# Optimization experiments

Hardware: AMD Instinct MI355X
Metric: run time of the kernel (lower is better)

The kernel has to match this reference:

```python
import jax, jax.numpy as jnp
import numpy as np

N_EMBD = 768
N_HEAD = 12
BLOCK_SIZE = 1024


def setup_inputs() -> dict:
    key = jax.random.key(0)
    ks = jax.random.split(key, 11)
    s = lambda fan_in: 1.0 / np.sqrt(fan_in)
    x = jax.random.normal(ks[0], (8, 1024, N_EMBD), dtype=jnp.float32)
    return {
        "x": x,
        "ln1_g": jnp.ones((N_EMBD,), jnp.float32),
        "ln1_b": jnp.zeros((N_EMBD,), jnp.float32),
        "w_attn": jax.random.normal(ks[1], (N_EMBD, 3 * N_EMBD), jnp.float32) * s(N_EMBD),
        "b_attn": jnp.zeros((3 * N_EMBD,), jnp.float32),
        "w_proj": jax.random.normal(ks[2], (N_EMBD, N_EMBD), jnp.float32) * s(N_EMBD),
        "b_proj": jnp.zeros((N_EMBD,), jnp.float32),
        "ln2_g": jnp.ones((N_EMBD,), jnp.float32),
        "ln2_b": jnp.zeros((N_EMBD,), jnp.float32),
        "w_fc": jax.random.normal(ks[3], (N_EMBD, 4 * N_EMBD), jnp.float32) * s(N_EMBD),
        "b_fc": jnp.zeros((4 * N_EMBD,), jnp.float32),
        "w_fc_proj": jax.random.normal(ks[4], (4 * N_EMBD, N_EMBD), jnp.float32) * s(4 * N_EMBD),
        "b_fc_proj": jnp.zeros((N_EMBD,), jnp.float32),
    }


def _layernorm(x, g, b, eps=1e-5):
    mu = jnp.mean(x, axis=-1, keepdims=True)
    var = jnp.var(x, axis=-1, keepdims=True)
    return (x - mu) * jax.lax.rsqrt(var + eps) * g + b


def _gelu_tanh(x):
    # GELU with tanh approximation (matches nn.GELU(approximate='tanh'))
    c = np.sqrt(2.0 / np.pi).astype(np.float32)
    return 0.5 * x * (1.0 + jnp.tanh(c * (x + 0.044715 * x * x * x)))


def _attn(x, w_attn, b_attn, w_proj, b_proj):
    B, T, C = x.shape
    hs = C // N_HEAD
    qkv = x @ w_attn + b_attn  # [B,T,3C]
    q, k, v = jnp.split(qkv, 3, axis=-1)
    # [B,T,C] -> [B,nh,T,hs]
    to_heads = lambda t: t.reshape(B, T, N_HEAD, hs).transpose(0, 2, 1, 3)
    q, k, v = to_heads(q), to_heads(k), to_heads(v)
    att = jnp.einsum('bhqd,bhkd->bhqk', q, k) * (1.0 / np.sqrt(hs))
    causal = jnp.tril(jnp.ones((T, T), bool))
    att = jnp.where(causal, att, -jnp.inf)
    att = jax.nn.softmax(att, axis=-1)
    y = jnp.einsum('bhqk,bhkd->bhqd', att, v)  # [B,nh,T,hs]
    y = y.transpose(0, 2, 1, 3).reshape(B, T, C)
    return y @ w_proj + b_proj


def reference(x, ln1_g, ln1_b, w_attn, b_attn, w_proj, b_proj,
              ln2_g, ln2_b, w_fc, b_fc, w_fc_proj, b_fc_proj):
    x = x + _attn(_layernorm(x, ln1_g, ln1_b), w_attn, b_attn, w_proj, b_proj)
    h = _layernorm(x, ln2_g, ln2_b)
    h = _gelu_tanh(h @ w_fc + b_fc) @ w_fc_proj + b_fc_proj
    return x + h
```

## Files before the change

### kernel.cpp

```cpp
#include <hip/hip_runtime.h>

typedef __bf16 bf16x8 __attribute__((ext_vector_type(8)));
typedef float  f32x4  __attribute__((ext_vector_type(4)));
typedef unsigned short ushort8 __attribute__((ext_vector_type(8)));

__device__ __forceinline__ unsigned short f2bf(float f) {
    unsigned u = __float_as_uint(f);
    u += 0x7FFFu + ((u >> 16) & 1u);
    return (unsigned short)(u >> 16);
}

__device__ __forceinline__ f32x4 mfma16x16x32(bf16x8 a, bf16x8 b, f32x4 c) {
    return __builtin_amdgcn_mfma_f32_16x16x32_bf16(a, b, c, 0, 0, 0);
}

__device__ __forceinline__ bf16x8 ld8(const unsigned short* p) {
    return __builtin_bit_cast(bf16x8, *(const ushort8*)p);
}

__device__ __forceinline__ float exp2_fast(float x) {
    float r; asm("v_exp_f32 %0, %1" : "=v"(r) : "v"(x)); return r;
}

__device__ __forceinline__ void glds16(const unsigned short* g, unsigned short* l) {
    __builtin_amdgcn_global_load_lds(
        (const __attribute__((address_space(1))) void*)g,
        (__attribute__((address_space(3))) void*)l, 16, 0, 0);
}

__device__ __forceinline__ float gelu_tanh(float x) {
    const float c = 0.7978845608028654f;
    float z = c * (x + 0.044715f * x * x * x);
    float e = __expf(2.f * z);
    float th = 1.f - 2.f / (e + 1.f);
    return 0.5f * x * (1.f + th);
}

#define N_EMBD 768
#define SEQ    1024
#define NHEAD  12
#define HS     64
#define MROWS  8192

__global__ __launch_bounds__(256) void tcast_kernel(const float* __restrict__ in,
                                                    unsigned short* __restrict__ out,
                                                    int K, int N) {
    __shared__ float tile[32][33];
    int nb = blockIdx.x * 32, kb = blockIdx.y * 32;
    int tx = threadIdx.x, ty = threadIdx.y;
#pragma unroll
    for (int i = 0; i < 4; i++) {
        int k = kb + ty + i * 8;
        tile[ty + i * 8][tx] = in[(size_t)k * N + nb + tx];
    }
    __syncthreads();
#pragma unroll
    for (int i = 0; i < 4; i++) {
        int n = nb + ty + i * 8;
        out[(size_t)n * K + kb + tx] = f2bf(tile[tx][ty + i * 8]);
    }
}

__global__ __launch_bounds__(256) void ln_kernel(const float* __restrict__ x,
                                                 const float* __restrict__ g,
                                                 const float* __restrict__ b,
                                                 unsigned short* __restrict__ out) {
    int row = blockIdx.x;
    const float* xr = x + (size_t)row * N_EMBD;
    float v[3], s = 0.f, s2 = 0.f;
#pragma unroll
    for (int i = 0; i < 3; i++) {
        v[i] = xr[threadIdx.x + i * 256];
        s += v[i]; s2 += v[i] * v[i];
    }
#pragma unroll
    for (int m = 1; m < 64; m <<= 1) { s += __shfl_xor(s, m); s2 += __shfl_xor(s2, m); }
    __shared__ float ps[4], ps2[4];
    int wid = threadIdx.x >> 6;
    if ((threadIdx.x & 63) == 0) { ps[wid] = s; ps2[wid] = s2; }
    __syncthreads();
    s  = ps[0] + ps[1] + ps[2] + ps[3];
    s2 = ps2[0] + ps2[1] + ps2[2] + ps2[3];
    float mu  = s * (1.f / N_EMBD);
    float var = s2 * (1.f / N_EMBD) - mu * mu;
    float inv = rsqrtf(var + 1e-5f);
#pragma unroll
    for (int i = 0; i < 3; i++) {
        int c = threadIdx.x + i * 256;
        out[(size_t)row * N_EMBD + c] = f2bf((v[i] - mu) * inv * g[c] + b[c]);
    }
}

template <int EPI, int WM>
__global__ __launch_bounds__(256) void gemm_bt_kernel(
    const unsigned short* __restrict__ A, const unsigned short* __restrict__ BT,
    const float* __restrict__ bias, const float* __restrict__ res,
    float* __restrict__ outF, unsigned short* __restrict__ outB,
    int M, int N, int K) {
    constexpr int BM = WM * 32;
    constexpr int ASZ = BM * 64;
    constexpr int BSZ = 128 * 64;
    __shared__ __attribute__((aligned(16))) unsigned short As[2 * ASZ];
    __shared__ __attribute__((aligned(16))) unsigned short Bs[2 * BSZ];
    const int gx = gridDim.x;
    const int slot = blockIdx.y * gx + blockIdx.x;
    const int chunk = (gx * gridDim.y) >> 3;
    const int logical = (slot & 7) * chunk + (slot >> 3);
    const int m0 = (logical / gx) * BM, n0 = (logical % gx) * 128;
    const int t = threadIdx.x, lane = t & 63, wid = t >> 6;
    const int wr = wid >> 1, wc = wid & 1;

    f32x4 acc[WM][4] = {};

    const int rrow = lane & 15, g = lane >> 4;
    const int swz8 = (rrow & 7) << 3;

    const int srow = t >> 3;
    const int scol = ((t & 7) ^ (srow & 7)) * 8;

    const int NT = K >> 6;
#pragma unroll
    for (int i = 0; i < WM; i++)
        glds16(&A[(size_t)(m0 + i * 32 + srow) * K + scol], &As[i * 2048 + wid * 512]);
#pragma unroll
    for (int i = 0; i < 4; i++)
        glds16(&BT[(size_t)(n0 + i * 32 + srow) * K + scol], &Bs[i * 2048 + wid * 512]);
    __syncthreads();

    int cur = 0;
    for (int kt = 0; kt < NT; ++kt) {
        if (kt + 1 < NT) {
            const int kk = (kt + 1) << 6;
            const int nb = (cur ^ 1);
#pragma unroll
            for (int i = 0; i < WM; i++)
                glds16(&A[(size_t)(m0 + i * 32 + srow) * K + kk + scol],
                       &As[nb * ASZ + i * 2048 + wid * 512]);
#pragma unroll
            for (int i = 0; i < 4; i++)
                glds16(&BT[(size_t)(n0 + i * 32 + srow) * K + kk + scol],
                       &Bs[nb * BSZ + i * 2048 + wid * 512]);
        }
        const unsigned short* ab = &As[cur * ASZ];
        const unsigned short* bb = &Bs[cur * BSZ];
#pragma unroll
        for (int s = 0; s < 2; s++) {
            bf16x8 af[WM], bfr[4];
#pragma unroll
            for (int i = 0; i < WM; i++) {
                int row = wr * (WM * 16) + i * 16 + rrow;
                af[i] = ld8(&ab[row * 64 + ((((s << 2) | g) << 3) ^ swz8)]);
            }
#pragma unroll
            for (int j = 0; j < 4; j++) {
                int row = wc * 64 + j * 16 + rrow;
                bfr[j] = ld8(&bb[row * 64 + ((((s << 2) | g) << 3) ^ swz8)]);
            }
#pragma unroll
            for (int i = 0; i < WM; i++)
#pragma unroll
                for (int j = 0; j < 4; j++) acc[i][j] = mfma16x16x32(af[i], bfr[j], acc[i][j]);
        }
        __syncthreads();
        cur ^= 1;
    }

    const int crow = g * 4, ccol = rrow;
#pragma unroll
    for (int i = 0; i < WM; i++) {
        int gr0 = m0 + wr * (WM * 16) + i * 16 + crow;
#pragma unroll
        for (int j = 0; j < 4; j++) {
            int gc = n0 + wc * 64 + j * 16 + ccol;
            float bv = bias[gc];
#pragma unroll
            for (int r = 0; r < 4; r++) {
                int gr = gr0 + r;
                float v = acc[i][j][r] + bv;
                if constexpr (EPI == 1) v = gelu_tanh(v);
                if constexpr (EPI == 2) {
                    outF[(size_t)gr * N + gc] = v + res[(size_t)gr * N + gc];
                } else {
                    outB[(size_t)gr * N + gc] = f2bf(v);
                }
            }
        }
    }
}

#define SCALE_LOG2E 0.18033688011112042f

__global__ __launch_bounds__(256, 4) void attn_kernel(const unsigned short* __restrict__ qkv,
                                                      unsigned short* __restrict__ yb) {
    const int slot = blockIdx.y * 8 + blockIdx.x;
    const int logical = (slot & 7) * 96 + (slot >> 3);
    const int p = logical & 7;
    const int bh = logical >> 3;
    const int b = bh / NHEAD, h = bh % NHEAD;
    const int t = threadIdx.x, lane = t & 63, wid = t >> 6;
    const int q0A = p * 64 + wid * 16, q0B = (15 - p) * 64 + wid * 16;
    const int ntA = p + 1, ntB = 16 - p;
    const int rrow = lane & 15, g = lane >> 4, kg8 = g * 8;

    __shared__ __attribute__((aligned(16))) unsigned short Ks[64 * 64];
    __shared__ __attribute__((aligned(16))) unsigned short Vt[64 * 88];
    __shared__ __attribute__((aligned(16))) unsigned short Ps[4][2][16 * 80];

    bf16x8 qfA[2], qfB[2];
    {
        size_t baseA = ((size_t)(b * SEQ + q0A + rrow)) * 2304 + h * HS;
        qfA[0] = ld8(&qkv[baseA + kg8]);
        qfA[1] = ld8(&qkv[baseA + 32 + kg8]);
        size_t baseB = ((size_t)(b * SEQ + q0B + rrow)) * 2304 + h * HS;
        qfB[0] = ld8(&qkv[baseB + kg8]);
        qfB[1] = ld8(&qkv[baseB + 32 + kg8]);
    }

    f32x4 yA[4] = {}, yB[4] = {};
    float lA[4] = {0.f, 0.f, 0.f, 0.f}, lB[4] = {0.f, 0.f, 0.f, 0.f};

    const int kr0 = t >> 3, kr1 = kr0 + 32;
    const int kc0 = ((t & 7) ^ (kr0 & 7)) * 8;
    const int vd = t & 63, vk = (t >> 6) * 16;

    unsigned short* PB = &Ps[wid][0][0];
    unsigned short* PA = &Ps[wid][1][0];
    const bf16x8 vones = __builtin_bit_cast(bf16x8,
        (ushort8){0x3F80, 0x3F80, 0x3F80, 0x3F80, 0x3F80, 0x3F80, 0x3F80, 0x3F80});

    for (int tt = 0; tt < ntB; tt++) {
        const int kv0 = tt * 64;
        const bool doA = (tt < ntA);
        const bool maskB = (tt == ntB - 1), maskA = (tt == ntA - 1);
        __syncthreads();
        glds16(&qkv[((size_t)(b * SEQ + kv0 + kr0)) * 2304 + 768 + h * HS + kc0], &Ks[wid * 512]);
        glds16(&qkv[((size_t)(b * SEQ + kv0 + kr1)) * 2304 + 768 + h * HS + kc0], &Ks[2048 + wid * 512]);
        ushort8 vlo, vhi;
#pragma unroll
        for (int i = 0; i < 8; i++)
            vlo[i] = qkv[((size_t)(b * SEQ + kv0 + vk + i)) * 2304 + 1536 + h * HS + vd];
#pragma unroll
        for (int i = 0; i < 8; i++)
            vhi[i] = qkv[((size_t)(b * SEQ + kv0 + vk + 8 + i)) * 2304 + 1536 + h * HS + vd];
        *(ushort8*)&Vt[vd * 88 + vk] = vlo;
        *(ushort8*)&Vt[vd * 88 + vk + 8] = vhi;
        __syncthreads();

        f32x4 sB[4], sA[4];
#pragma unroll
        for (int ct = 0; ct < 4; ct++) {
            const int j = ct * 16 + rrow;
            const unsigned short* kr = &Ks[j * 64];
            bf16x8 k0 = ld8(&kr[((g    ) ^ (j & 7)) * 8]);
            bf16x8 k1 = ld8(&kr[((g + 4) ^ (j & 7)) * 8]);
            f32x4 zB = {};
            zB = mfma16x16x32(qfB[0], k0, zB);
            zB = mfma16x16x32(qfB[1], k1, zB);
            sB[ct] = zB;
            if (doA) {
                f32x4 zA = {};
                zA = mfma16x16x32(qfA[0], k0, zA);
                zA = mfma16x16x32(qfA[1], k1, zA);
                sA[ct] = zA;
            }
        }
        const int qrbB = q0B + g * 4, qrbA = q0A + g * 4;
#pragma unroll
        for (int ct = 0; ct < 4; ct++) {
            const int j = ct * 16 + rrow, jj = kv0 + j;
#pragma unroll
            for (int r = 0; r < 4; r++) {
                float v = sB[ct][r] * SCALE_LOG2E;
                if (maskB && jj > qrbB + r) v = -1e30f;
                const int q = g * 4 + r;
                PB[q * 80 + (j ^ ((q & 7) << 3))] = f2bf(exp2_fast(v));
            }
        }
        if (doA) {
#pragma unroll
            for (int ct = 0; ct < 4; ct++) {
                const int j = ct * 16 + rrow, jj = kv0 + j;
#pragma unroll
                for (int r = 0; r < 4; r++) {
                    float v = sA[ct][r] * SCALE_LOG2E;
                    if (maskA && jj > qrbA + r) v = -1e30f;
                    const int q = g * 4 + r;
                    PA[q * 80 + (j ^ ((q & 7) << 3))] = f2bf(exp2_fast(v));
                }
            }
        }
        asm volatile("s_waitcnt lgkmcnt(0)" ::: "memory");
        __builtin_amdgcn_sched_barrier(0);
        const int sw = (rrow & 7) << 3;
        bf16x8 paB0 = ld8(&PB[rrow * 80 + ((kg8     ) ^ sw)]);
        bf16x8 paB1 = ld8(&PB[rrow * 80 + ((kg8 + 32) ^ sw)]);
        bf16x8 paA0, paA1;
        if (doA) {
            paA0 = ld8(&PA[rrow * 80 + ((kg8     ) ^ sw)]);
            paA1 = ld8(&PA[rrow * 80 + ((kg8 + 32) ^ sw)]);
        }
        __builtin_amdgcn_s_setprio(1);
        f32x4 ssB = {};
        ssB = mfma16x16x32(paB0, vones, ssB);
        ssB = mfma16x16x32(paB1, vones, ssB);
#pragma unroll
        for (int r = 0; r < 4; r++) lB[r] += ssB[r];
        if (doA) {
            f32x4 ssA = {};
            ssA = mfma16x16x32(paA0, vones, ssA);
            ssA = mfma16x16x32(paA1, vones, ssA);
#pragma unroll
            for (int r = 0; r < 4; r++) lA[r] += ssA[r];
        }
#pragma unroll
        for (int dt = 0; dt < 4; dt++) {
            const unsigned short* vr = &Vt[(dt * 16 + rrow) * 88];
            bf16x8 v0 = ld8(&vr[kg8]);
            bf16x8 v1 = ld8(&vr[kg8 + 32]);
            yB[dt] = mfma16x16x32(paB0, v0, yB[dt]);
            yB[dt] = mfma16x16x32(paB1, v1, yB[dt]);
            if (doA) {
                yA[dt] = mfma16x16x32(paA0, v0, yA[dt]);
                yA[dt] = mfma16x16x32(paA1, v1, yA[dt]);
            }
        }
        __builtin_amdgcn_s_setprio(0);
    }

#pragma unroll
    for (int dt = 0; dt < 4; dt++)
#pragma unroll
        for (int r = 0; r < 4; r++) {
            int col = h * HS + dt * 16 + rrow;
            yb[((size_t)(b * SEQ + q0B + g * 4 + r)) * N_EMBD + col] = f2bf(yB[dt][r] / lB[r]);
            yb[((size_t)(b * SEQ + q0A + g * 4 + r)) * N_EMBD + col] = f2bf(yA[dt][r] / lA[r]);
        }
}

extern "C" void kernel_launch(void* const* d_in, const int* in_sizes, int n_in,
                              void* d_out, int out_size, void* d_ws, size_t ws_size,
                              hipStream_t stream) {
    const float* x        = (const float*)d_in[0];
    const float* ln1_g    = (const float*)d_in[1];
    const float* ln1_b    = (const float*)d_in[2];
    const float* w_attn   = (const float*)d_in[3];
    const float* b_attn   = (const float*)d_in[4];
    const float* w_proj   = (const float*)d_in[5];
    const float* b_proj   = (const float*)d_in[6];
    const float* ln2_g    = (const float*)d_in[7];
    const float* ln2_b    = (const float*)d_in[8];
    const float* w_fc     = (const float*)d_in[9];
    const float* b_fc     = (const float*)d_in[10];
    const float* w_fcp    = (const float*)d_in[11];
    const float* b_fcp    = (const float*)d_in[12];
    float* out = (float*)d_out;

    unsigned short* ws = (unsigned short*)d_ws;
    unsigned short* wT_attn = ws;
    unsigned short* wT_proj = wT_attn + 2304 * 768;
    unsigned short* wT_fc   = wT_proj + 768 * 768;
    unsigned short* wT_fcp  = wT_fc   + 3072 * 768;
    unsigned short* xb      = wT_fcp  + 768 * 3072;
    unsigned short* qkv     = xb      + (size_t)MROWS * 768;
    unsigned short* yb      = qkv     + (size_t)MROWS * 2304;
    unsigned short* act     = qkv;
    float* x2 = (float*)(yb + (size_t)MROWS * 768);

    dim3 tb(32, 8);
    tcast_kernel<<<dim3(2304 / 32, 768 / 32), tb, 0, stream>>>(w_attn, wT_attn, 768, 2304);
    tcast_kernel<<<dim3(768 / 32, 768 / 32),  tb, 0, stream>>>(w_proj, wT_proj, 768, 768);
    tcast_kernel<<<dim3(3072 / 32, 768 / 32), tb, 0, stream>>>(w_fc,   wT_fc,   768, 3072);
    tcast_kernel<<<dim3(768 / 32, 3072 / 32), tb, 0, stream>>>(w_fcp,  wT_fcp,  3072, 768);

    ln_kernel<<<MROWS, 256, 0, stream>>>(x, ln1_g, ln1_b, xb);
    gemm_bt_kernel<0, 4><<<dim3(2304 / 128, MROWS / 128), 256, 0, stream>>>(
        xb, wT_attn, b_attn, nullptr, nullptr, qkv, MROWS, 2304, 768);
    attn_kernel<<<dim3(8, 96), 256, 0, stream>>>(qkv, yb);
    gemm_bt_kernel<2, 2><<<dim3(768 / 128, MROWS / 64), 256, 0, stream>>>(
        yb, wT_proj, b_proj, x, x2, nullptr, MROWS, 768, 768);
    ln_kernel<<<MROWS, 256, 0, stream>>>(x2, ln2_g, ln2_b, xb);
    gemm_bt_kernel<1, 4><<<dim3(3072 / 128, MROWS / 128), 256, 0, stream>>>(
        xb, wT_fc, b_fc, nullptr, nullptr, act, MROWS, 3072, 768);
    gemm_bt_kernel<2, 2><<<dim3(768 / 128, MROWS / 64), 256, 0, stream>>>(
        act, wT_fcp, b_fcp, x2, out, nullptr, MROWS, 768, 3072);
}
```

Baseline: 260.0 us.

## Add 256x256-tile 8-wave GEMM kernel for QKV and FC projections

Adds a new bf16 MFMA GEMM kernel that uses 256x256 output tiles, 512 threads and double-buffered swizzled LDS. Its main loop interleaves quarter-tile loads for the next K steps with MFMA phases, using barriers and setprio. The QKV and FC1 GEMMs now use it instead of the 128x128 kernel, aiming for more data reuse per block and better overlap of loads with compute. The cost is fewer blocks (e.g. 9x32 for QKV), which can leave CUs underused and lowers occupancy; the kernel uses 128KB of LDS.

Result: slower. 272.8 us (+4.9%).

```diff
diff --git a/kernel.cpp b/kernel.cpp
--- a/kernel.cpp
+++ b/kernel.cpp
@@ -88,6 +88,164 @@
     for (int i = 0; i < 3; i++) {
         int c = threadIdx.x + i * 256;
         out[(size_t)row * N_EMBD + c] = f2bf((v[i] - mu) * inv * g[c] + b[c]);
+    }
+}
+
+template <int EPI>
+__global__ __launch_bounds__(512, 2) void gemm256_kernel(
+    const unsigned short* __restrict__ A, const unsigned short* __restrict__ BT,
+    const float* __restrict__ bias, unsigned short* __restrict__ outB,
+    int M, int N, int K) {
+    __shared__ __attribute__((aligned(16))) unsigned short As[2][16384];
+    __shared__ __attribute__((aligned(16))) unsigned short Bs[2][16384];
+    const int gx = gridDim.x;
+    const int slot = blockIdx.y * gx + blockIdx.x;
+    const int chunk = (gx * gridDim.y) >> 3;
+    const int logical = (slot & 7) * chunk + (slot >> 3);
+    const int m0 = (logical / gx) * 256, n0 = (logical % gx) * 256;
+    const int t = threadIdx.x, lane = t & 63, w = t >> 6;
+    const int wr = w >> 2, wc = w & 3;
+    const int rrow = lane & 15, g = lane >> 4;
+
+    f32x4 acc[8][4] = {};
+
+    const int sr0 = t >> 3;
+    const int sr1 = 64 + (t >> 3);
+    const int sc0 = ((t & 7) ^ (sr0 & 7)) * 8;
+    const int sc1 = ((t & 7) ^ (sr1 & 7)) * 8;
+    const int NT = K >> 6;
+
+    auto stageA = [&](int kt, int bf, int hf) {
+        const unsigned short* base = A + (size_t)(m0 + hf * 128) * K + (kt << 6);
+        glds16(base + (size_t)sr0 * K + sc0, &As[bf][hf * 8192 + w * 512]);
+        glds16(base + (size_t)sr1 * K + sc1, &As[bf][hf * 8192 + 4096 + w * 512]);
+    };
+    auto stageB = [&](int kt, int bf, int hf) {
+        const unsigned short* base = BT + (size_t)(n0 + hf * 128) * K + (kt << 6);
+        glds16(base + (size_t)sr0 * K + sc0, &Bs[bf][hf * 8192 + w * 512]);
+        glds16(base + (size_t)sr1 * K + sc1, &Bs[bf][hf * 8192 + 4096 + w * 512]);
+    };
+
+    stageA(0, 0, 0); stageB(0, 0, 0); stageB(0, 0, 1); stageA(0, 0, 1);
+    if (NT > 1) { stageA(1, 1, 0); stageB(1, 1, 0); }
+    asm volatile("s_waitcnt vmcnt(4)" ::: "memory");
+    __builtin_amdgcn_sched_barrier(0);
+    __builtin_amdgcn_s_barrier();
+
+    bf16x8 af[4][2], b0[2][2], b1[2][2];
+
+    for (int kt = 0; kt < NT; ++kt) {
+        const int cb = kt & 1, nb = cb ^ 1;
+        const unsigned short* ab = As[cb];
+        const unsigned short* bb = Bs[cb];
+
+#pragma unroll
+        for (int i = 0; i < 4; i++)
+#pragma unroll
+            for (int s = 0; s < 2; s++) {
+                int row = wr * 128 + i * 16 + rrow;
+                af[i][s] = ld8(&ab[row * 64 + ((((s << 2) | g) ^ (row & 7)) << 3)]);
+            }
+#pragma unroll
+        for (int j = 0; j < 2; j++)
+#pragma unroll
+            for (int s = 0; s < 2; s++) {
+                int row = wc * 64 + j * 16 + rrow;
+                b0[j][s] = ld8(&bb[row * 64 + ((((s << 2) | g) ^ (row & 7)) << 3)]);
+            }
+        if (kt + 1 < NT) stageB(kt + 1, nb, 1);
+        __builtin_amdgcn_s_barrier();
+        asm volatile("s_waitcnt lgkmcnt(0)" ::: "memory");
+        __builtin_amdgcn_sched_barrier(0);
+        __builtin_amdgcn_s_setprio(1);
+#pragma unroll
+        for (int i = 0; i < 4; i++)
+#pragma unroll
+            for (int j = 0; j < 2; j++)
+#pragma unroll
+                for (int s = 0; s < 2; s++)
+                    acc[i][j] = mfma16x16x32(af[i][s], b0[j][s], acc[i][j]);
+        __builtin_amdgcn_s_setprio(0);
+        __builtin_amdgcn_s_barrier();
+
+#pragma unroll
+        for (int j = 0; j < 2; j++)
+#pragma unroll
+            for (int s = 0; s < 2; s++) {
+                int row = wc * 64 + (2 + j) * 16 + rrow;
+                b1[j][s] = ld8(&bb[row * 64 + ((((s << 2) | g) ^ (row & 7)) << 3)]);
+            }
+        if (kt + 1 < NT) stageA(kt + 1, nb, 1);
+        __builtin_amdgcn_s_barrier();
+        asm volatile("s_waitcnt lgkmcnt(0)" ::: "memory");
+        __builtin_amdgcn_sched_barrier(0);
+        __builtin_amdgcn_s_setprio(1);
+#pragma unroll
+        for (int i = 0; i < 4; i++)
+#pragma unroll
+            for (int j = 0; j < 2; j++)
+#pragma unroll
+                for (int s = 0; s < 2; s++)
+                    acc[i][2 + j] = mfma16x16x32(af[i][s], b1[j][s], acc[i][2 + j]);
+        __builtin_amdgcn_s_setprio(0);
+        __builtin_amdgcn_s_barrier();
+
+#pragma unroll
+        for (int i = 0; i < 4; i++)
+#pragma unroll
+            for (int s = 0; s < 2; s++) {
+                int row = wr * 128 + 64 + i * 16 + rrow;
+                af[i][s] = ld8(&ab[row * 64 + ((((s << 2) | g) ^ (row & 7)) << 3)]);
+            }
+        if (kt + 2 < NT) stageA(kt + 2, cb, 0);
+        __builtin_amdgcn_s_barrier();
+        asm volatile("s_waitcnt lgkmcnt(0)" ::: "memory");
+        __builtin_amdgcn_sched_barrier(0);
+        __builtin_amdgcn_s_setprio(1);
+#pragma unroll
+        for (int i = 0; i < 4; i++)
+#pragma unroll
+            for (int j = 0; j < 2; j++)
+#pragma unroll
+                for (int s = 0; s < 2; s++)
+                    acc[4 + i][2 + j] = mfma16x16x32(af[i][s], b1[j][s], acc[4 + i][2 + j]);
+        __builtin_amdgcn_s_setprio(0);
+        __builtin_amdgcn_s_barrier();
+
+        if (kt + 2 < NT) stageB(kt + 2, cb, 0);
+        __builtin_amdgcn_s_barrier();
+        __builtin_amdgcn_s_setprio(1);
+#pragma unroll
+        for (int i = 0; i < 4; i++)
+#pragma unroll
+            for (int j = 0; j < 2; j++)
+#pragma unroll
+                for (int s = 0; s < 2; s++)
+                    acc[4 + i][j] = mfma16x16x32(af[i][s], b0[j][s], acc[4 + i][j]);
+        __builtin_amdgcn_s_setprio(0);
+        if (kt + 2 < NT) {
+            asm volatile("s_waitcnt vmcnt(4)" ::: "memory");
+        } else {
+            asm volatile("s_waitcnt vmcnt(0)" ::: "memory");
+        }
+        __builtin_amdgcn_sched_barrier(0);
+        __builtin_amdgcn_s_barrier();
+    }
+
+#pragma unroll
+    for (int mf = 0; mf < 8; mf++) {
+        int gr0 = m0 + wr * 128 + mf * 16 + g * 4;
+#pragma unroll
+        for (int nf = 0; nf < 4; nf++) {
+            int gc = n0 + wc * 64 + nf * 16 + rrow;
+            float bv = bias[gc];
+#pragma unroll
+            for (int r = 0; r < 4; r++) {
+                float v = acc[mf][nf][r] + bv;
+                if constexpr (EPI == 1) v = gelu_tanh(v);
+                outB[(size_t)(gr0 + r) * N + gc] = f2bf(v);
+            }
+        }
     }
 }
 
@@ -373,14 +531,14 @@
     tcast_kernel<<<dim3(768 / 32, 3072 / 32), tb, 0, stream>>>(w_fcp,  wT_fcp,  3072, 768);
 
     ln_kernel<<<MROWS, 256, 0, stream>>>(x, ln1_g, ln1_b, xb);
-    gemm_bt_kernel<0, 4><<<dim3(2304 / 128, MROWS / 128), 256, 0, stream>>>(
-        xb, wT_attn, b_attn, nullptr, nullptr, qkv, MROWS, 2304, 768);
+    gemm256_kernel<0><<<dim3(2304 / 256, MROWS / 256), 512, 0, stream>>>(
+        xb, wT_attn, b_attn, qkv, MROWS, 2304, 768);
     attn_kernel<<<dim3(8, 96), 256, 0, stream>>>(qkv, yb);
     gemm_bt_kernel<2, 2><<<dim3(768 / 128, MROWS / 64), 256, 0, stream>>>(
         yb, wT_proj, b_proj, x, x2, nullptr, MROWS, 768, 768);
     ln_kernel<<<MROWS, 256, 0, stream>>>(x2, ln2_g, ln2_b, xb);
-    gemm_bt_kernel<1, 4><<<dim3(3072 / 128, MROWS / 128), 256, 0, stream>>>(
-        xb, wT_fc, b_fc, nullptr, nullptr, act, MROWS, 3072, 768);
+    gemm256_kernel<1><<<dim3(3072 / 256, MROWS / 256), 512, 0, stream>>>(
+        xb, wT_fc, b_fc, act, MROWS, 3072, 768);
     gemm_bt_kernel<2, 2><<<dim3(768 / 128, MROWS / 64), 256, 0, stream>>>(
         act, wT_fcp, b_fcp, x2, out, nullptr, MROWS, 768, 3072);
 }
```
